# Kernel tuning notes

Hardware: AMD Instinct MI355X
Metric: run time of the kernel (lower is better)

Reference implementation:

```python
import jax, jax.numpy as jnp
import numpy as np

N_NODES = 100000
N_EDGES = 600000
N_GRAPHS = 5000
IN_DIM = 11
HID = 128
EDGE_DIM = 3
N_REST = 4  # layers 1..4
BN_EPS = 1e-5


def setup_inputs() -> dict:
    key = jax.random.key(0)
    ks = iter(jax.random.split(key, 40))
    s = 0.05
    inp = {}
    inp['x'] = jax.random.normal(next(ks), (N_NODES, IN_DIM), dtype=jnp.float32)
    inp['edge_attr'] = jax.random.normal(next(ks), (N_EDGES, EDGE_DIM), dtype=jnp.float32)
    # layer 0 (input_dim -> hidden)
    inp['e_w0'] = jax.random.normal(next(ks), (EDGE_DIM, IN_DIM), dtype=jnp.float32) * s
    inp['e_b0'] = jnp.zeros((IN_DIM,), jnp.float32)
    inp['w1_0'] = jax.random.normal(next(ks), (IN_DIM, HID), dtype=jnp.float32) * s
    inp['b1_0'] = jnp.zeros((HID,), jnp.float32)
    inp['w2_0'] = jax.random.normal(next(ks), (HID, HID), dtype=jnp.float32) * s
    inp['b2_0'] = jnp.zeros((HID,), jnp.float32)
    inp['gamma0'] = jnp.ones((HID,), jnp.float32)
    inp['beta0'] = jnp.zeros((HID,), jnp.float32)
    inp['eps0'] = jnp.zeros((), jnp.float32)
    # layers 1..4 stacked
    inp['e_w'] = jax.random.normal(next(ks), (N_REST, EDGE_DIM, HID), dtype=jnp.float32) * s
    inp['e_b'] = jnp.zeros((N_REST, HID), jnp.float32)
    inp['w1'] = jax.random.normal(next(ks), (N_REST, HID, HID), dtype=jnp.float32) * s
    inp['b1'] = jnp.zeros((N_REST, HID), jnp.float32)
    inp['w2'] = jax.random.normal(next(ks), (N_REST, HID, HID), dtype=jnp.float32) * s
    inp['b2'] = jnp.zeros((N_REST, HID), jnp.float32)
    inp['gamma'] = jnp.ones((N_REST, HID), jnp.float32)
    inp['beta'] = jnp.zeros((N_REST, HID), jnp.float32)
    inp['eps_r'] = jnp.zeros((N_REST,), jnp.float32)
    # head MLP
    inp['hw1'] = jax.random.normal(next(ks), (HID, HID), dtype=jnp.float32) * s
    inp['hb1'] = jnp.zeros((HID,), jnp.float32)
    inp['hw2'] = jax.random.normal(next(ks), (HID, HID), dtype=jnp.float32) * s
    inp['hb2'] = jnp.zeros((HID,), jnp.float32)
    inp['hw3'] = jax.random.normal(next(ks), (HID, 1), dtype=jnp.float32) * s
    inp['hb3'] = jnp.zeros((1,), jnp.float32)
    # graph structure (int constants)
    inp['edge_index'] = jax.random.randint(next(ks), (2, N_EDGES), 0, N_NODES, dtype=jnp.int32)
    inp['batch'] = jnp.sort(jax.random.randint(next(ks), (N_NODES,), 0, N_GRAPHS, dtype=jnp.int32))
    return inp


def _gine_layer(x, src, dst, edge_attr, e_w, e_b, eps, w1, b1, w2, b2, gamma, beta):
    # message = relu(x_j + Linear(edge_attr)); aggregate = scatter-add on dst
    msg = jax.nn.relu(x[src] + edge_attr @ e_w + e_b)            # [E, d]
    aggr = jax.ops.segment_sum(msg, dst, num_segments=N_NODES)  # [N, d]
    h = (1.0 + eps) * x + aggr
    h = jax.nn.relu(h @ w1 + b1) @ w2 + b2                       # GIN MLP
    mu = h.mean(axis=0)
    var = h.var(axis=0)  # biased, as torch BN training-mode normalization
    h = (h - mu) * jax.lax.rsqrt(var + BN_EPS) * gamma + beta
    return jax.nn.relu(h)


def reference(x, edge_attr, e_w0, e_b0, w1_0, b1_0, w2_0, b2_0, gamma0, beta0, eps0,
              e_w, e_b, w1, b1, w2, b2, gamma, beta, eps_r,
              hw1, hb1, hw2, hb2, hw3, hb3, edge_index, batch):
    src, dst = edge_index[0], edge_index[1]
    # layer 0: input_dim -> hidden, no residual (dims differ)
    h = _gine_layer(x, src, dst, edge_attr, e_w0, e_b0, eps0,
                    w1_0, b1_0, w2_0, b2_0, gamma0, beta0)
    # layers 1..4: hidden -> hidden, with residual
    for i in range(N_REST):
        h_res = h
        h = _gine_layer(h, src, dst, edge_attr, e_w[i], e_b[i], eps_r[i],
                        w1[i], b1[i], w2[i], b2[i], gamma[i], beta[i])
        h = h + h_res
    # global mean pool per graph
    sums = jax.ops.segment_sum(h, batch, num_segments=N_GRAPHS)
    cnts = jax.ops.segment_sum(jnp.ones((h.shape[0],), h.dtype), batch, num_segments=N_GRAPHS)
    pooled = sums / jnp.maximum(cnts, 1.0)[:, None]
    # head MLP (dropout = eval no-op)
    z = jax.nn.relu(pooled @ hw1 + hb1)
    z = jax.nn.relu(z @ hw2 + hb2)
    return z @ hw3 + hb3
```

## Files before the change

### kernel.cpp

```cpp
#include <hip/hip_runtime.h>
#include <hip/hip_fp16.h>

#define N_NODES 100000
#define N_EDGES 600000
#define N_GRAPHS 5000
#define IN_DIM 11
#define HID 128
#define NREST 4
#define BN_EPS 1e-5f
#define SCAN_BS 256
#define NBLK ((N_NODES + SCAN_BS - 1) / SCAN_BS)
#define WSLOT 16384

typedef __bf16 bf16x8 __attribute__((ext_vector_type(8)));
typedef float f32x4 __attribute__((ext_vector_type(4)));

__device__ inline bf16x8 as_bf16x8(uint4 u) { return __builtin_bit_cast(bf16x8, u); }

__device__ inline void split_bf16(float x, unsigned short& hi, unsigned short& lo) {
    unsigned int b = __float_as_uint(x);
    hi = (unsigned short)(b >> 16);
    float rem = x - __uint_as_float(b & 0xFFFF0000u);
    lo = (unsigned short)(__float_as_uint(rem) >> 16);
}

__device__ inline uint4 pack8(const unsigned short* h) {
    uint4 u;
    u.x = (unsigned)h[0] | ((unsigned)h[1] << 16);
    u.y = (unsigned)h[2] | ((unsigned)h[3] << 16);
    u.z = (unsigned)h[4] | ((unsigned)h[5] << 16);
    u.w = (unsigned)h[6] | ((unsigned)h[7] << 16);
    return u;
}

__global__ void k_zero(int* deg, int* gstart, int* gend, float* stats) {
    int i = blockIdx.x * 256 + threadIdx.x;
    if (i < N_NODES) deg[i] = 0;
    if (i < N_GRAPHS) { gstart[i] = 0; gend[i] = 0; }
    if (i < 5 * 2 * HID) stats[i] = 0.f;
}

__global__ void k_deg(const int* __restrict__ ei, int* __restrict__ deg) {
    int e = blockIdx.x * 256 + threadIdx.x;
    if (e < N_EDGES) atomicAdd(&deg[ei[N_EDGES + e]], 1);
}

__global__ void k_scan_a(const int* __restrict__ deg, int* __restrict__ rowstart,
                         int* __restrict__ bsum) {
    __shared__ int sh[SCAN_BS];
    int t = threadIdx.x, i = blockIdx.x * SCAN_BS + t;
    int v = (i < N_NODES) ? deg[i] : 0;
    sh[t] = v;
    __syncthreads();
    for (int off = 1; off < SCAN_BS; off <<= 1) {
        int add = (t >= off) ? sh[t - off] : 0;
        __syncthreads();
        sh[t] += add;
        __syncthreads();
    }
    if (i < N_NODES) rowstart[i] = sh[t] - v;
    if (t == SCAN_BS - 1) bsum[blockIdx.x] = sh[t];
}

__global__ void k_scan_b(const int* __restrict__ bsum, int* __restrict__ boff) {
    __shared__ int sh[512];
    int t = threadIdx.x;
    int v = (t < NBLK) ? bsum[t] : 0;
    sh[t] = v;
    __syncthreads();
    for (int off = 1; off < 512; off <<= 1) {
        int add = (t >= off) ? sh[t - off] : 0;
        __syncthreads();
        sh[t] += add;
        __syncthreads();
    }
    if (t < NBLK) boff[t] = sh[t] - v;
}

__global__ void k_scan_c(int* __restrict__ rowstart, const int* __restrict__ boff,
                         int* __restrict__ cur) {
    int i = blockIdx.x * 256 + threadIdx.x;
    if (i < N_NODES) {
        int v = rowstart[i] + boff[i / SCAN_BS];
        rowstart[i] = v;
        cur[i] = v;
    }
    if (i == 0) rowstart[N_NODES] = N_EDGES;
}

__global__ void k_fill(const int* __restrict__ ei, const float* __restrict__ ea,
                       int* __restrict__ cur, uint4* __restrict__ csr_pack) {
    int e = blockIdx.x * 256 + threadIdx.x;
    if (e < N_EDGES) {
        int d = ei[N_EDGES + e];
        int p = atomicAdd(&cur[d], 1);
        uint4 pk;
        pk.x = (unsigned)ei[e];
        pk.y = __float_as_uint(ea[3 * e + 0]);
        pk.z = __float_as_uint(ea[3 * e + 1]);
        pk.w = __float_as_uint(ea[3 * e + 2]);
        csr_pack[p] = pk;
    }
}

__global__ void k_pack(const float* __restrict__ w1_0, const float* __restrict__ w2_0,
                       const float* __restrict__ w1, const float* __restrict__ w2,
                       unsigned short* __restrict__ Whi, unsigned short* __restrict__ Wlo) {
    int bid = blockIdx.x;
    int slot = bid >> 5;
    int kc = (bid >> 3) & 3, cb = bid & 7;
    int lane = threadIdx.x;
    const float* src;
    int K;
    if (slot == 0) { src = w1_0; K = IN_DIM; }
    else if (slot == 1) { src = w2_0; K = HID; }
    else if (slot < 6) { src = w1 + (size_t)(slot - 2) * HID * HID; K = HID; }
    else { src = w2 + (size_t)(slot - 6) * HID * HID; K = HID; }
    int col = cb * 16 + (lane & 15);
    int kbase = kc * 32 + 8 * (lane >> 4);
    unsigned short hi[8], lo[8];
#pragma unroll
    for (int j = 0; j < 8; ++j) {
        int k = kbase + j;
        float v = (k < K) ? src[(size_t)k * HID + col] : 0.f;
        split_bf16(v, hi[j], lo[j]);
    }
    size_t base = ((size_t)bid * 64 + lane) * 8;
    *(uint4*)(Whi + base) = pack8(hi);
    *(uint4*)(Wlo + base) = pack8(lo);
}

__global__ void k_agg0(const float* __restrict__ x, const int* __restrict__ rowstart,
                       const uint4* __restrict__ csr_pack,
                       const float* __restrict__ ew, const float* __restrict__ eb,
                       const float* __restrict__ epsp, float* __restrict__ Z0) {
    int wave = (blockIdx.x * blockDim.x + threadIdx.x) >> 6;
    int lane = threadIdx.x & 63;
    if (wave >= N_NODES) return;
    int n = wave;
    int slot = lane >> 4;
    int c = lane & 15;
    int cc = (c < IN_DIM) ? c : 0;
    float w0 = ew[cc], w1 = ew[IN_DIM + cc], w2 = ew[2 * IN_DIM + cc];
    float bb = eb[cc];
    float acc = 0.f;
    int i0 = rowstart[n], i1 = rowstart[n + 1];
    for (int i = i0 + slot; i < i1; i += 4) {
        uint4 pk = csr_pack[i];
        int s = (int)pk.x;
        float m = x[s * IN_DIM + cc] + __uint_as_float(pk.y) * w0 +
                  __uint_as_float(pk.z) * w1 + __uint_as_float(pk.w) * w2 + bb;
        acc += fmaxf(m, 0.f);
    }
    acc += __shfl_xor(acc, 16, 64);
    acc += __shfl_xor(acc, 32, 64);
    if (lane < IN_DIM) {
        float epsv = 1.0f + epsp[0];
        Z0[n * IN_DIM + lane] = epsv * x[n * IN_DIM + lane] + acc;
    }
}

__global__ __launch_bounds__(256, 4) void k_agg128(
        const __half* __restrict__ hh, const int* __restrict__ rowstart,
        const uint4* __restrict__ csr_pack,
        const float* __restrict__ ew, const float* __restrict__ eb,
        const float* __restrict__ epsp, int layer, float* __restrict__ Z) {
    int wave = (blockIdx.x * blockDim.x + threadIdx.x) >> 6;
    int lane = threadIdx.x & 63;
    if (wave >= N_NODES) return;
    int n = wave;
    int slot = lane >> 4;
    int c = (lane & 15) * 8;
    float4 w0a = *(const float4*)(ew + 0 * HID + c), w0b = *(const float4*)(ew + 0 * HID + c + 4);
    float4 w1a = *(const float4*)(ew + 1 * HID + c), w1b = *(const float4*)(ew + 1 * HID + c + 4);
    float4 w2a = *(const float4*)(ew + 2 * HID + c), w2b = *(const float4*)(ew + 2 * HID + c + 4);
    float4 bba = *(const float4*)(eb + c),           bbb = *(const float4*)(eb + c + 4);
    float a0 = 0.f, a1 = 0.f, a2 = 0.f, a3 = 0.f, a4 = 0.f, a5 = 0.f, a6 = 0.f, a7 = 0.f;
    int i0 = rowstart[n], i1 = rowstart[n + 1];
    for (int i = i0 + slot; i < i1; i += 4) {
        uint4 pk = csr_pack[i];
        int s = (int)pk.x;
        float ea0 = __uint_as_float(pk.y);
        float ea1 = __uint_as_float(pk.z);
        float ea2 = __uint_as_float(pk.w);
        uint4 hv = *(const uint4*)(hh + (size_t)s * HID + c);
        float2 f0 = __half22float2(__builtin_bit_cast(__half2, hv.x));
        float2 f1 = __half22float2(__builtin_bit_cast(__half2, hv.y));
        float2 f2 = __half22float2(__builtin_bit_cast(__half2, hv.z));
        float2 f3 = __half22float2(__builtin_bit_cast(__half2, hv.w));
        a0 += fmaxf(f0.x + ea0 * w0a.x + ea1 * w1a.x + ea2 * w2a.x + bba.x, 0.f);
        a1 += fmaxf(f0.y + ea0 * w0a.y + ea1 * w1a.y + ea2 * w2a.y + bba.y, 0.f);
        a2 += fmaxf(f1.x + ea0 * w0a.z + ea1 * w1a.z + ea2 * w2a.z + bba.z, 0.f);
        a3 += fmaxf(f1.y + ea0 * w0a.w + ea1 * w1a.w + ea2 * w2a.w + bba.w, 0.f);
        a4 += fmaxf(f2.x + ea0 * w0b.x + ea1 * w1b.x + ea2 * w2b.x + bbb.x, 0.f);
        a5 += fmaxf(f2.y + ea0 * w0b.y + ea1 * w1b.y + ea2 * w2b.y + bbb.y, 0.f);
        a6 += fmaxf(f3.x + ea0 * w0b.z + ea1 * w1b.z + ea2 * w2b.z + bbb.z, 0.f);
        a7 += fmaxf(f3.y + ea0 * w0b.w + ea1 * w1b.w + ea2 * w2b.w + bbb.w, 0.f);
    }
#pragma unroll
    for (int m = 16; m <= 32; m <<= 1) {
        a0 += __shfl_xor(a0, m, 64); a1 += __shfl_xor(a1, m, 64);
        a2 += __shfl_xor(a2, m, 64); a3 += __shfl_xor(a3, m, 64);
        a4 += __shfl_xor(a4, m, 64); a5 += __shfl_xor(a5, m, 64);
        a6 += __shfl_xor(a6, m, 64); a7 += __shfl_xor(a7, m, 64);
    }
    if (slot == 0) {
        float epsv = 1.0f + epsp[layer];
        uint4 hv = *(const uint4*)(hh + (size_t)n * HID + c);
        float2 f0 = __half22float2(__builtin_bit_cast(__half2, hv.x));
        float2 f1 = __half22float2(__builtin_bit_cast(__half2, hv.y));
        float2 f2 = __half22float2(__builtin_bit_cast(__half2, hv.z));
        float2 f3 = __half22float2(__builtin_bit_cast(__half2, hv.w));
        float4 za, zb;
        za.x = epsv * f0.x + a0; za.y = epsv * f0.y + a1;
        za.z = epsv * f1.x + a2; za.w = epsv * f1.y + a3;
        zb.x = epsv * f2.x + a4; zb.y = epsv * f2.y + a5;
        zb.z = epsv * f3.x + a6; zb.w = epsv * f3.y + a7;
        *(float4*)(Z + (size_t)n * HID + c) = za;
        *(float4*)(Z + (size_t)n * HID + c + 4) = zb;
    }
}

template <int K1>
__global__ __launch_bounds__(512, 8) void k_mlp(const float* Zin,
        const unsigned short* __restrict__ W1hi, const unsigned short* __restrict__ W1lo,
        const unsigned short* __restrict__ W2hi, const unsigned short* __restrict__ W2lo,
        const float* __restrict__ B1, const float* __restrict__ B2,
        float* Hpre, float* __restrict__ stats) {
    constexpr int KC1 = (K1 == 128) ? 4 : 1;
    __shared__ __align__(16) unsigned short ahi[4 * 4 * 64 * 8];
    __shared__ __align__(16) unsigned short alo[4 * 4 * 64 * 8];
    __shared__ float red[1024];
    const int tid = threadIdx.x;
    const int w = tid >> 6;
    const int l = tid & 63;
    const int row0 = blockIdx.x * 64;

    if (K1 == 128) {
#pragma unroll
        for (int it = 0; it < 2; ++it) {
            int s = tid + it * 512;
            int lane = s & 63, kc = (s >> 6) & 3, wr = s >> 8;
            int r = row0 + wr * 16 + (lane & 15);
            int k0 = kc * 32 + 8 * (lane >> 4);
            float v[8];
            if (r < N_NODES) {
                *(float4*)(v) = *(const float4*)(Zin + (size_t)r * 128 + k0);
                *(float4*)(v + 4) = *(const float4*)(Zin + (size_t)r * 128 + k0 + 4);
            } else {
#pragma unroll
                for (int j = 0; j < 8; ++j) v[j] = 0.f;
            }
            unsigned short h[8], q[8];
#pragma unroll
            for (int j = 0; j < 8; ++j) split_bf16(v[j], h[j], q[j]);
            *(uint4*)(ahi + (size_t)s * 8) = pack8(h);
            *(uint4*)(alo + (size_t)s * 8) = pack8(q);
        }
    } else {
        if (tid < 256) {
            int lane = tid & 63, wr = tid >> 6;
            int r = row0 + wr * 16 + (lane & 15);
            int k0 = 8 * (lane >> 4);
            float v[8];
#pragma unroll
            for (int j = 0; j < 8; ++j) {
                int k = k0 + j;
                v[j] = (r < N_NODES && k < IN_DIM) ? Zin[(size_t)r * IN_DIM + k] : 0.f;
            }
            unsigned short h[8], q[8];
#pragma unroll
            for (int j = 0; j < 8; ++j) split_bf16(v[j], h[j], q[j]);
            size_t s = (size_t)(wr * 4 + 0) * 64 + lane;
            *(uint4*)(ahi + s * 8) = pack8(h);
            *(uint4*)(alo + s * 8) = pack8(q);
        }
    }
    __syncthreads();

    const int cb = w;
    const f32x4 zf = {0.f, 0.f, 0.f, 0.f};

    f32x4 acc[4];
#pragma unroll
    for (int wr = 0; wr < 4; ++wr) acc[wr] = zf;

#pragma unroll
    for (int kc = 0; kc < KC1; ++kc) {
        bf16x8 bh = as_bf16x8(*(const uint4*)(W1hi + ((size_t)(kc * 8 + cb) * 64 + l) * 8));
        bf16x8 bl = as_bf16x8(*(const uint4*)(W1lo + ((size_t)(kc * 8 + cb) * 64 + l) * 8));
#pragma unroll
        for (int wr = 0; wr < 4; ++wr) {
            bf16x8 a_h = as_bf16x8(*(const uint4*)(ahi + ((size_t)(wr * 4 + kc) * 64 + l) * 8));
            bf16x8 a_l = as_bf16x8(*(const uint4*)(alo + ((size_t)(wr * 4 + kc) * 64 + l) * 8));
            acc[wr] = __builtin_amdgcn_mfma_f32_16x16x32_bf16(a_h, bh, acc[wr], 0, 0, 0);
            acc[wr] = __builtin_amdgcn_mfma_f32_16x16x32_bf16(a_l, bh, acc[wr], 0, 0, 0);
            acc[wr] = __builtin_amdgcn_mfma_f32_16x16x32_bf16(a_h, bl, acc[wr], 0, 0, 0);
        }
    }
    __syncthreads();

    {
        float b1c = B1[cb * 16 + (l & 15)];
        int cc = l & 15;
        int g = 2 * (w & 1) + (cc >> 3);
        int j = cc & 7;
        int kc2 = w >> 1;
        int rl0 = (l >> 4) * 4;
#pragma unroll
        for (int wr = 0; wr < 4; ++wr) {
#pragma unroll
            for (int r = 0; r < 4; ++r) {
                float t = fmaxf(acc[wr][r] + b1c, 0.f);
                unsigned short th, tq;
                split_bf16(t, th, tq);
                int l2 = g * 16 + rl0 + r;
                int off = ((wr * 4 + kc2) * 64 + l2) * 8 + j;
                ahi[off] = th;
                alo[off] = tq;
            }
        }
    }
    __syncthreads();

    f32x4 acc2[4];
#pragma unroll
    for (int wr = 0; wr < 4; ++wr) acc2[wr] = zf;

#pragma unroll
    for (int kc = 0; kc < 4; ++kc) {
        bf16x8 bh = as_bf16x8(*(const uint4*)(W2hi + ((size_t)(kc * 8 + cb) * 64 + l) * 8));
        bf16x8 bl = as_bf16x8(*(const uint4*)(W2lo + ((size_t)(kc * 8 + cb) * 64 + l) * 8));
#pragma unroll
        for (int wr = 0; wr < 4; ++wr) {
            bf16x8 a_h = as_bf16x8(*(const uint4*)(ahi + ((size_t)(wr * 4 + kc) * 64 + l) * 8));
            bf16x8 a_l = as_bf16x8(*(const uint4*)(alo + ((size_t)(wr * 4 + kc) * 64 + l) * 8));
            acc2[wr] = __builtin_amdgcn_mfma_f32_16x16x32_bf16(a_h, bh, acc2[wr], 0, 0, 0);
            acc2[wr] = __builtin_amdgcn_mfma_f32_16x16x32_bf16(a_l, bh, acc2[wr], 0, 0, 0);
            acc2[wr] = __builtin_amdgcn_mfma_f32_16x16x32_bf16(a_h, bl, acc2[wr], 0, 0, 0);
        }
    }

    {
        float b2c = B2[cb * 16 + (l & 15)];
        int col = cb * 16 + (l & 15);
        float s0 = 0.f, q0 = 0.f;
#pragma unroll
        for (int wr = 0; wr < 4; ++wr) {
#pragma unroll
            for (int r = 0; r < 4; ++r) {
                int grow = row0 + wr * 16 + (l >> 4) * 4 + r;
                if (grow < N_NODES) {
                    float o = acc2[wr][r] + b2c;
                    Hpre[(size_t)grow * 128 + col] = o;
                    s0 += o;
                    q0 += o * o;
                }
            }
        }
        red[w * 64 + l] = s0;
        red[512 + w * 64 + l] = q0;
    }
    __syncthreads();
    if (tid < 128) {
        int b = (tid >> 4) * 64 + (tid & 15);
        float ss = red[b] + red[b + 16] + red[b + 32] + red[b + 48];
        float qq = red[512 + b] + red[512 + b + 16] + red[512 + b + 32] + red[512 + b + 48];
        atomicAdd(&stats[tid], ss);
        atomicAdd(&stats[128 + tid], qq);
    }
}

__global__ void k_bn(const float* __restrict__ Hpre, const float* __restrict__ stats,
                     const float* __restrict__ gamma, const float* __restrict__ beta,
                     const __half* __restrict__ hprev, __half* __restrict__ hout) {
    int idx = blockIdx.x * 256 + threadIdx.x;
    const float invN = 1.f / (float)N_NODES;
    int cg = (idx & 15) * 8;
    const float* hp = Hpre + (size_t)idx * 8;
    float4 v0 = *(const float4*)(hp);
    float4 v1 = *(const float4*)(hp + 4);
    float4 s0a = *(const float4*)(stats + cg);
    float4 s0b = *(const float4*)(stats + cg + 4);
    float4 s1a = *(const float4*)(stats + 128 + cg);
    float4 s1b = *(const float4*)(stats + 128 + cg + 4);
    float4 ga = *(const float4*)(gamma + cg);
    float4 gb = *(const float4*)(gamma + cg + 4);
    float4 ba = *(const float4*)(beta + cg);
    float4 bb = *(const float4*)(beta + cg + 4);
    float vv[8] = {v0.x, v0.y, v0.z, v0.w, v1.x, v1.y, v1.z, v1.w};
    float sm[8] = {s0a.x, s0a.y, s0a.z, s0a.w, s0b.x, s0b.y, s0b.z, s0b.w};
    float sq[8] = {s1a.x, s1a.y, s1a.z, s1a.w, s1b.x, s1b.y, s1b.z, s1b.w};
    float gg[8] = {ga.x, ga.y, ga.z, ga.w, gb.x, gb.y, gb.z, gb.w};
    float be[8] = {ba.x, ba.y, ba.z, ba.w, bb.x, bb.y, bb.z, bb.w};
    float o[8];
#pragma unroll
    for (int j = 0; j < 8; ++j) {
        float mu = sm[j] * invN, var = sq[j] * invN - mu * mu;
        o[j] = fmaxf((vv[j] - mu) * rsqrtf(var + BN_EPS) * gg[j] + be[j], 0.f);
    }
    if (hprev) {
        uint4 pv = *(const uint4*)(hprev + (size_t)idx * 8);
        float2 r0 = __half22float2(__builtin_bit_cast(__half2, pv.x));
        float2 r1 = __half22float2(__builtin_bit_cast(__half2, pv.y));
        float2 r2 = __half22float2(__builtin_bit_cast(__half2, pv.z));
        float2 r3 = __half22float2(__builtin_bit_cast(__half2, pv.w));
        o[0] += r0.x; o[1] += r0.y; o[2] += r1.x; o[3] += r1.y;
        o[4] += r2.x; o[5] += r2.y; o[6] += r3.x; o[7] += r3.y;
    }
    uint4 st;
    st.x = __builtin_bit_cast(unsigned int, __floats2half2_rn(o[0], o[1]));
    st.y = __builtin_bit_cast(unsigned int, __floats2half2_rn(o[2], o[3]));
    st.z = __builtin_bit_cast(unsigned int, __floats2half2_rn(o[4], o[5]));
    st.w = __builtin_bit_cast(unsigned int, __floats2half2_rn(o[6], o[7]));
    *(uint4*)(hout + (size_t)idx * 8) = st;
}

__global__ void k_bounds(const int* __restrict__ batch, int* __restrict__ gstart,
                         int* __restrict__ gend) {
    int r = blockIdx.x * 256 + threadIdx.x;
    if (r >= N_NODES) return;
    int b = batch[r];
    if (r == 0 || batch[r - 1] != b) gstart[b] = r;
    if (r == N_NODES - 1 || batch[r + 1] != b) gend[b] = r + 1;
}

__global__ void k_pool(const __half* __restrict__ hh, const int* __restrict__ gstart,
                       const int* __restrict__ gend, float* __restrict__ pooled) {
    int wave = (blockIdx.x * blockDim.x + threadIdx.x) >> 6;
    int lane = threadIdx.x & 63;
    if (wave >= N_GRAPHS) return;
    int g = wave;
    int c = lane * 2;
    int a = gstart[g], b = gend[g];
    float ax = 0.f, ay = 0.f;
    for (int r = a; r < b; ++r) {
        __half2 v = *(const __half2*)(hh + (size_t)r * HID + c);
        float2 f = __half22float2(v);
        ax += f.x;
        ay += f.y;
    }
    float d = fmaxf((float)(b - a), 1.f);
    float2 o;
    o.x = ax / d;
    o.y = ay / d;
    *(float2*)(pooled + (size_t)g * HID + c) = o;
}

__global__ void k_head(const float* __restrict__ pooled, const float* __restrict__ hw1,
                       const float* __restrict__ hb1, const float* __restrict__ hw2,
                       const float* __restrict__ hb2, const float* __restrict__ hw3,
                       const float* __restrict__ hb3, float* __restrict__ out) {
    __shared__ float ps[2][128];
    __shared__ float t1s[2][128];
    __shared__ float red[256];
    int tid = threadIdx.x;
    int rr = tid >> 7, c = tid & 127;
    int row = blockIdx.x * 2 + rr;
    ps[rr][c] = pooled[(size_t)row * 128 + c];
    __syncthreads();
    float a = hb1[c];
    for (int k = 0; k < 128; ++k) a = fmaf(ps[rr][k], hw1[k * 128 + c], a);
    t1s[rr][c] = fmaxf(a, 0.f);
    __syncthreads();
    float b = hb2[c];
    for (int k = 0; k < 128; ++k) b = fmaf(t1s[rr][k], hw2[k * 128 + c], b);
    b = fmaxf(b, 0.f);
    red[tid] = b * hw3[c];
    for (int s = 64; s > 0; s >>= 1) {
        __syncthreads();
        if (c < s) red[tid] += red[tid + s];
    }
    __syncthreads();
    if (c == 0) out[row] = red[tid] + hb3[0];
}

extern "C" void kernel_launch(void* const* d_in, const int* in_sizes, int n_in,
                              void* d_out, int out_size, void* d_ws, size_t ws_size,
                              hipStream_t stream) {
    const float* x = (const float*)d_in[0];
    const float* edge_attr = (const float*)d_in[1];
    const float* e_w0 = (const float*)d_in[2];
    const float* e_b0 = (const float*)d_in[3];
    const float* w1_0 = (const float*)d_in[4];
    const float* b1_0 = (const float*)d_in[5];
    const float* w2_0 = (const float*)d_in[6];
    const float* b2_0 = (const float*)d_in[7];
    const float* gamma0 = (const float*)d_in[8];
    const float* beta0 = (const float*)d_in[9];
    const float* eps0 = (const float*)d_in[10];
    const float* e_w = (const float*)d_in[11];
    const float* e_b = (const float*)d_in[12];
    const float* w1 = (const float*)d_in[13];
    const float* b1 = (const float*)d_in[14];
    const float* w2 = (const float*)d_in[15];
    const float* b2 = (const float*)d_in[16];
    const float* gamma = (const float*)d_in[17];
    const float* beta = (const float*)d_in[18];
    const float* eps_r = (const float*)d_in[19];
    const float* hw1 = (const float*)d_in[20];
    const float* hb1 = (const float*)d_in[21];
    const float* hw2 = (const float*)d_in[22];
    const float* hb2 = (const float*)d_in[23];
    const float* hw3 = (const float*)d_in[24];
    const float* hb3 = (const float*)d_in[25];
    const int* edge_index = (const int*)d_in[26];
    const int* batch = (const int*)d_in[27];
    float* out = (float*)d_out;

    float* wsf = (float*)d_ws;
    size_t off = 0;
    float* ZB = wsf + off;     off += (size_t)N_NODES * HID;
    float* Z0 = wsf + off;     off += (size_t)N_NODES * IN_DIM + 4;
    float* pooled = wsf + off; off += (size_t)N_GRAPHS * HID;
    float* stats = wsf + off;  off += 5 * 2 * HID;
    __half* hhA = (__half*)(wsf + off); off += (size_t)N_NODES * HID / 2;
    __half* hhB = (__half*)(wsf + off); off += (size_t)N_NODES * HID / 2;
    int* ib = (int*)(wsf + off);
    uint4* csr_pack = (uint4*)ib;
    size_t io = 4 * (size_t)N_EDGES;
    int* deg = ib + io;      io += N_NODES;
    int* rowstart = ib + io; io += N_NODES + 4;
    int* cur = ib + io;      io += N_NODES;
    int* gstart = ib + io;   io += N_GRAPHS;
    int* gend = ib + io;     io += N_GRAPHS;
    int* bsum = ib + io;     io += 512;
    int* boff = ib + io;     io += 512;
    unsigned short* Whi = (unsigned short*)(ib + io);
    unsigned short* Wlo = Whi + 10 * WSLOT;

    const int EB = (N_EDGES + 255) / 256;
    const int NB = (N_NODES + 255) / 256;
    const int MLPB = (N_NODES + 63) / 64;
    const int BNB = (N_NODES * HID / 8) / 256;

    k_zero<<<NB, 256, 0, stream>>>(deg, gstart, gend, stats);
    k_pack<<<320, 64, 0, stream>>>(w1_0, w2_0, w1, w2, Whi, Wlo);

    k_deg<<<EB, 256, 0, stream>>>(edge_index, deg);
    k_scan_a<<<NBLK, SCAN_BS, 0, stream>>>(deg, rowstart, bsum);
    k_scan_b<<<1, 512, 0, stream>>>(bsum, boff);
    k_scan_c<<<NB, 256, 0, stream>>>(rowstart, boff, cur);
    k_fill<<<EB, 256, 0, stream>>>(edge_index, edge_attr, cur, csr_pack);

    k_agg0<<<(N_NODES * 64) / 256, 256, 0, stream>>>(x, rowstart, csr_pack, e_w0,
                                                     e_b0, eps0, Z0);
    k_mlp<IN_DIM><<<MLPB, 512, 0, stream>>>(Z0, Whi + 0 * WSLOT, Wlo + 0 * WSLOT,
                                            Whi + 1 * WSLOT, Wlo + 1 * WSLOT,
                                            b1_0, b2_0, ZB, stats);
    k_bn<<<BNB, 256, 0, stream>>>(ZB, stats, gamma0, beta0, (const __half*)nullptr, hhA);

    __half* hcur = hhA;
    __half* hnxt = hhB;
    for (int i = 0; i < NREST; ++i) {
        k_agg128<<<(N_NODES * 64) / 256, 256, 0, stream>>>(
            hcur, rowstart, csr_pack, e_w + (size_t)i * 3 * HID,
            e_b + (size_t)i * HID, eps_r, i, ZB);
        k_mlp<HID><<<MLPB, 512, 0, stream>>>(ZB, Whi + (size_t)(2 + i) * WSLOT,
                                             Wlo + (size_t)(2 + i) * WSLOT,
                                             Whi + (size_t)(6 + i) * WSLOT,
                                             Wlo + (size_t)(6 + i) * WSLOT,
                                             b1 + (size_t)i * HID, b2 + (size_t)i * HID,
                                             ZB, stats + (size_t)(i + 1) * 2 * HID);
        k_bn<<<BNB, 256, 0, stream>>>(ZB, stats + (size_t)(i + 1) * 2 * HID,
                                      gamma + (size_t)i * HID, beta + (size_t)i * HID,
                                      hcur, hnxt);
        __half* t = hcur; hcur = hnxt; hnxt = t;
    }

    k_bounds<<<NB, 256, 0, stream>>>(batch, gstart, gend);
    k_pool<<<(N_GRAPHS * 64) / 256, 256, 0, stream>>>(hcur, gstart, gend, pooled);
    k_head<<<N_GRAPHS / 2, 256, 0, stream>>>(pooled, hw1, hb1, hw2, hb2, hw3, hb3, out);
}
```

Before: 942.6 us.

## Fuse neighbor aggregation into MLP kernel, staging aggregated rows in LDS

Aggregation kernels are merged into the MLP kernel. Each block of 512 threads aggregates its 64 nodes (8 per wave) and writes the split bf16 fragments straight into shared memory, so the fp32 Z intermediate no longer makes a round trip through global memory. The MLP output is also staged through LDS and written with coalesced float4 stores. The cost is less parallelism during the gather phase, since each wave now processes 8 nodes serially. Launch bounds also drop to 4 blocks per CU, which may reduce latency hiding for the irregular gathers.

```diff
diff --git a/kernel.cpp b/kernel.cpp
--- a/kernel.cpp
+++ b/kernel.cpp
@@ -11,6 +11,7 @@
 #define SCAN_BS 256
 #define NBLK ((N_NODES + SCAN_BS - 1) / SCAN_BS)
 #define WSLOT 16384
+#define FB ((N_NODES + 63) / 64)
 
 typedef __bf16 bf16x8 __attribute__((ext_vector_type(8)));
 typedef float f32x4 __attribute__((ext_vector_type(4)));
@@ -130,150 +131,132 @@
     *(uint4*)(Wlo + base) = pack8(lo);
 }
 
-__global__ void k_agg0(const float* __restrict__ x, const int* __restrict__ rowstart,
-                       const uint4* __restrict__ csr_pack,
-                       const float* __restrict__ ew, const float* __restrict__ eb,
-                       const float* __restrict__ epsp, float* __restrict__ Z0) {
-    int wave = (blockIdx.x * blockDim.x + threadIdx.x) >> 6;
-    int lane = threadIdx.x & 63;
-    if (wave >= N_NODES) return;
-    int n = wave;
-    int slot = lane >> 4;
-    int c = lane & 15;
-    int cc = (c < IN_DIM) ? c : 0;
-    float w0 = ew[cc], w1 = ew[IN_DIM + cc], w2 = ew[2 * IN_DIM + cc];
-    float bb = eb[cc];
-    float acc = 0.f;
-    int i0 = rowstart[n], i1 = rowstart[n + 1];
-    for (int i = i0 + slot; i < i1; i += 4) {
-        uint4 pk = csr_pack[i];
-        int s = (int)pk.x;
-        float m = x[s * IN_DIM + cc] + __uint_as_float(pk.y) * w0 +
-                  __uint_as_float(pk.z) * w1 + __uint_as_float(pk.w) * w2 + bb;
-        acc += fmaxf(m, 0.f);
-    }
-    acc += __shfl_xor(acc, 16, 64);
-    acc += __shfl_xor(acc, 32, 64);
-    if (lane < IN_DIM) {
-        float epsv = 1.0f + epsp[0];
-        Z0[n * IN_DIM + lane] = epsv * x[n * IN_DIM + lane] + acc;
-    }
-}
-
-__global__ __launch_bounds__(256, 4) void k_agg128(
-        const __half* __restrict__ hh, const int* __restrict__ rowstart,
-        const uint4* __restrict__ csr_pack,
+template <int K1>
+__global__ __launch_bounds__(512, 4) void k_fused(
+        const float* __restrict__ x, const __half* __restrict__ hh,
+        const int* __restrict__ rowstart, const uint4* __restrict__ csr_pack,
         const float* __restrict__ ew, const float* __restrict__ eb,
-        const float* __restrict__ epsp, int layer, float* __restrict__ Z) {
-    int wave = (blockIdx.x * blockDim.x + threadIdx.x) >> 6;
-    int lane = threadIdx.x & 63;
-    if (wave >= N_NODES) return;
-    int n = wave;
-    int slot = lane >> 4;
-    int c = (lane & 15) * 8;
-    float4 w0a = *(const float4*)(ew + 0 * HID + c), w0b = *(const float4*)(ew + 0 * HID + c + 4);
-    float4 w1a = *(const float4*)(ew + 1 * HID + c), w1b = *(const float4*)(ew + 1 * HID + c + 4);
-    float4 w2a = *(const float4*)(ew + 2 * HID + c), w2b = *(const float4*)(ew + 2 * HID + c + 4);
-    float4 bba = *(const float4*)(eb + c),           bbb = *(const float4*)(eb + c + 4);
-    float a0 = 0.f, a1 = 0.f, a2 = 0.f, a3 = 0.f, a4 = 0.f, a5 = 0.f, a6 = 0.f, a7 = 0.f;
-    int i0 = rowstart[n], i1 = rowstart[n + 1];
-    for (int i = i0 + slot; i < i1; i += 4) {
-        uint4 pk = csr_pack[i];
-        int s = (int)pk.x;
-        float ea0 = __uint_as_float(pk.y);
-        float ea1 = __uint_as_float(pk.z);
-        float ea2 = __uint_as_float(pk.w);
-        uint4 hv = *(const uint4*)(hh + (size_t)s * HID + c);
-        float2 f0 = __half22float2(__builtin_bit_cast(__half2, hv.x));
-        float2 f1 = __half22float2(__builtin_bit_cast(__half2, hv.y));
-        float2 f2 = __half22float2(__builtin_bit_cast(__half2, hv.z));
-        float2 f3 = __half22float2(__builtin_bit_cast(__half2, hv.w));
-        a0 += fmaxf(f0.x + ea0 * w0a.x + ea1 * w1a.x + ea2 * w2a.x + bba.x, 0.f);
-        a1 += fmaxf(f0.y + ea0 * w0a.y + ea1 * w1a.y + ea2 * w2a.y + bba.y, 0.f);
-        a2 += fmaxf(f1.x + ea0 * w0a.z + ea1 * w1a.z + ea2 * w2a.z + bba.z, 0.f);
-        a3 += fmaxf(f1.y + ea0 * w0a.w + ea1 * w1a.w + ea2 * w2a.w + bba.w, 0.f);
-        a4 += fmaxf(f2.x + ea0 * w0b.x + ea1 * w1b.x + ea2 * w2b.x + bbb.x, 0.f);
-        a5 += fmaxf(f2.y + ea0 * w0b.y + ea1 * w1b.y + ea2 * w2b.y + bbb.y, 0.f);
-        a6 += fmaxf(f3.x + ea0 * w0b.z + ea1 * w1b.z + ea2 * w2b.z + bbb.z, 0.f);
-        a7 += fmaxf(f3.y + ea0 * w0b.w + ea1 * w1b.w + ea2 * w2b.w + bbb.w, 0.f);
-    }
-#pragma unroll
-    for (int m = 16; m <= 32; m <<= 1) {
-        a0 += __shfl_xor(a0, m, 64); a1 += __shfl_xor(a1, m, 64);
-        a2 += __shfl_xor(a2, m, 64); a3 += __shfl_xor(a3, m, 64);
-        a4 += __shfl_xor(a4, m, 64); a5 += __shfl_xor(a5, m, 64);
-        a6 += __shfl_xor(a6, m, 64); a7 += __shfl_xor(a7, m, 64);
-    }
-    if (slot == 0) {
-        float epsv = 1.0f + epsp[layer];
-        uint4 hv = *(const uint4*)(hh + (size_t)n * HID + c);
-        float2 f0 = __half22float2(__builtin_bit_cast(__half2, hv.x));
-        float2 f1 = __half22float2(__builtin_bit_cast(__half2, hv.y));
-        float2 f2 = __half22float2(__builtin_bit_cast(__half2, hv.z));
-        float2 f3 = __half22float2(__builtin_bit_cast(__half2, hv.w));
-        float4 za, zb;
-        za.x = epsv * f0.x + a0; za.y = epsv * f0.y + a1;
-        za.z = epsv * f1.x + a2; za.w = epsv * f1.y + a3;
-        zb.x = epsv * f2.x + a4; zb.y = epsv * f2.y + a5;
-        zb.z = epsv * f3.x + a6; zb.w = epsv * f3.y + a7;
-        *(float4*)(Z + (size_t)n * HID + c) = za;
-        *(float4*)(Z + (size_t)n * HID + c + 4) = zb;
-    }
-}
-
-template <int K1>
-__global__ __launch_bounds__(512, 8) void k_mlp(const float* Zin,
+        const float* __restrict__ epsp, int layer,
         const unsigned short* __restrict__ W1hi, const unsigned short* __restrict__ W1lo,
         const unsigned short* __restrict__ W2hi, const unsigned short* __restrict__ W2lo,
         const float* __restrict__ B1, const float* __restrict__ B2,
-        float* Hpre, float* __restrict__ stats) {
+        float* __restrict__ Hpre, float* __restrict__ stats) {
     constexpr int KC1 = (K1 == 128) ? 4 : 1;
-    __shared__ __align__(16) unsigned short ahi[4 * 4 * 64 * 8];
-    __shared__ __align__(16) unsigned short alo[4 * 4 * 64 * 8];
+    __shared__ __align__(16) unsigned short afrag[2 * 4 * 4 * 64 * 8];
     __shared__ float red[1024];
+    unsigned short* ahi = afrag;
+    unsigned short* alo = afrag + 8192;
     const int tid = threadIdx.x;
     const int w = tid >> 6;
     const int l = tid & 63;
     const int row0 = blockIdx.x * 64;
+    const float epsv = 1.0f + epsp[layer];
+    const int slot = l >> 4;
+
+    if (K1 == 11) {
+        if (tid < 256) {
+            int off = ((tid >> 6) * 256 + (tid & 63)) * 8;
+            uint4 z = {0, 0, 0, 0};
+            *(uint4*)(ahi + off) = z;
+            *(uint4*)(alo + off) = z;
+        }
+        __syncthreads();
+    }
 
     if (K1 == 128) {
-#pragma unroll
-        for (int it = 0; it < 2; ++it) {
-            int s = tid + it * 512;
-            int lane = s & 63, kc = (s >> 6) & 3, wr = s >> 8;
-            int r = row0 + wr * 16 + (lane & 15);
-            int k0 = kc * 32 + 8 * (lane >> 4);
-            float v[8];
-            if (r < N_NODES) {
-                *(float4*)(v) = *(const float4*)(Zin + (size_t)r * 128 + k0);
-                *(float4*)(v + 4) = *(const float4*)(Zin + (size_t)r * 128 + k0 + 4);
-            } else {
-#pragma unroll
-                for (int j = 0; j < 8; ++j) v[j] = 0.f;
-            }
-            unsigned short h[8], q[8];
-#pragma unroll
-            for (int j = 0; j < 8; ++j) split_bf16(v[j], h[j], q[j]);
-            *(uint4*)(ahi + (size_t)s * 8) = pack8(h);
-            *(uint4*)(alo + (size_t)s * 8) = pack8(q);
+        int cg = (l & 15) * 8;
+        float4 w0a = *(const float4*)(ew + 0 * HID + cg), w0b = *(const float4*)(ew + 0 * HID + cg + 4);
+        float4 w1a = *(const float4*)(ew + 1 * HID + cg), w1b = *(const float4*)(ew + 1 * HID + cg + 4);
+        float4 w2a = *(const float4*)(ew + 2 * HID + cg), w2b = *(const float4*)(ew + 2 * HID + cg + 4);
+        float4 bba = *(const float4*)(eb + cg),           bbb = *(const float4*)(eb + cg + 4);
+        for (int nn = 0; nn < 8; ++nn) {
+            int rl = w * 8 + nn;
+            int n = row0 + rl;
+            bool valid = (n < N_NODES);
+            float a0 = 0.f, a1 = 0.f, a2 = 0.f, a3 = 0.f, a4 = 0.f, a5 = 0.f, a6 = 0.f, a7 = 0.f;
+            if (valid) {
+                int i0 = rowstart[n], i1 = rowstart[n + 1];
+                for (int i = i0 + slot; i < i1; i += 4) {
+                    uint4 pk = csr_pack[i];
+                    int s = (int)pk.x;
+                    float ea0 = __uint_as_float(pk.y);
+                    float ea1 = __uint_as_float(pk.z);
+                    float ea2 = __uint_as_float(pk.w);
+                    uint4 hv = *(const uint4*)(hh + (size_t)s * HID + cg);
+                    float2 f0 = __half22float2(__builtin_bit_cast(__half2, hv.x));
+                    float2 f1 = __half22float2(__builtin_bit_cast(__half2, hv.y));
+                    float2 f2 = __half22float2(__builtin_bit_cast(__half2, hv.z));
+                    float2 f3 = __half22float2(__builtin_bit_cast(__half2, hv.w));
+                    a0 += fmaxf(f0.x + ea0 * w0a.x + ea1 * w1a.x + ea2 * w2a.x + bba.x, 0.f);
+                    a1 += fmaxf(f0.y + ea0 * w0a.y + ea1 * w1a.y + ea2 * w2a.y + bba.y, 0.f);
+                    a2 += fmaxf(f1.x + ea0 * w0a.z + ea1 * w1a.z + ea2 * w2a.z + bba.z, 0.f);
+                    a3 += fmaxf(f1.y + ea0 * w0a.w + ea1 * w1a.w + ea2 * w2a.w + bba.w, 0.f);
+                    a4 += fmaxf(f2.x + ea0 * w0b.x + ea1 * w1b.x + ea2 * w2b.x + bbb.x, 0.f);
+                    a5 += fmaxf(f2.y + ea0 * w0b.y + ea1 * w1b.y + ea2 * w2b.y + bbb.y, 0.f);
+                    a6 += fmaxf(f3.x + ea0 * w0b.z + ea1 * w1b.z + ea2 * w2b.z + bbb.z, 0.f);
+                    a7 += fmaxf(f3.y + ea0 * w0b.w + ea1 * w1b.w + ea2 * w2b.w + bbb.w, 0.f);
+                }
+            }
+#pragma unroll
+            for (int m = 16; m <= 32; m <<= 1) {
+                a0 += __shfl_xor(a0, m, 64); a1 += __shfl_xor(a1, m, 64);
+                a2 += __shfl_xor(a2, m, 64); a3 += __shfl_xor(a3, m, 64);
+                a4 += __shfl_xor(a4, m, 64); a5 += __shfl_xor(a5, m, 64);
+                a6 += __shfl_xor(a6, m, 64); a7 += __shfl_xor(a7, m, 64);
+            }
+            if (slot == 0) {
+                int lc = l & 15;
+                float z[8] = {0.f, 0.f, 0.f, 0.f, 0.f, 0.f, 0.f, 0.f};
+                if (valid) {
+                    uint4 hv = *(const uint4*)(hh + (size_t)n * HID + cg);
+                    float2 f0 = __half22float2(__builtin_bit_cast(__half2, hv.x));
+                    float2 f1 = __half22float2(__builtin_bit_cast(__half2, hv.y));
+                    float2 f2 = __half22float2(__builtin_bit_cast(__half2, hv.z));
+                    float2 f3 = __half22float2(__builtin_bit_cast(__half2, hv.w));
+                    z[0] = epsv * f0.x + a0; z[1] = epsv * f0.y + a1;
+                    z[2] = epsv * f1.x + a2; z[3] = epsv * f1.y + a3;
+                    z[4] = epsv * f2.x + a4; z[5] = epsv * f2.y + a5;
+                    z[6] = epsv * f3.x + a6; z[7] = epsv * f3.y + a7;
+                }
+                unsigned short h8[8], q8[8];
+#pragma unroll
+                for (int j = 0; j < 8; ++j) split_bf16(z[j], h8[j], q8[j]);
+                int sidx = ((rl >> 4) * 4 + (lc >> 2)) * 64 + (lc & 3) * 16 + (rl & 15);
+                *(uint4*)(ahi + (size_t)sidx * 8) = pack8(h8);
+                *(uint4*)(alo + (size_t)sidx * 8) = pack8(q8);
+            }
         }
     } else {
-        if (tid < 256) {
-            int lane = tid & 63, wr = tid >> 6;
-            int r = row0 + wr * 16 + (lane & 15);
-            int k0 = 8 * (lane >> 4);
-            float v[8];
-#pragma unroll
-            for (int j = 0; j < 8; ++j) {
-                int k = k0 + j;
-                v[j] = (r < N_NODES && k < IN_DIM) ? Zin[(size_t)r * IN_DIM + k] : 0.f;
-            }
-            unsigned short h[8], q[8];
-#pragma unroll
-            for (int j = 0; j < 8; ++j) split_bf16(v[j], h[j], q[j]);
-            size_t s = (size_t)(wr * 4 + 0) * 64 + lane;
-            *(uint4*)(ahi + s * 8) = pack8(h);
-            *(uint4*)(alo + s * 8) = pack8(q);
+        int c = l & 15;
+        int cc = (c < IN_DIM) ? c : 0;
+        float w0 = ew[cc], w1 = ew[IN_DIM + cc], w2 = ew[2 * IN_DIM + cc];
+        float bb = eb[cc];
+        for (int nn = 0; nn < 8; ++nn) {
+            int rl = w * 8 + nn;
+            int n = row0 + rl;
+            bool valid = (n < N_NODES);
+            float acc = 0.f;
+            if (valid) {
+                int i0 = rowstart[n], i1 = rowstart[n + 1];
+                for (int i = i0 + slot; i < i1; i += 4) {
+                    uint4 pk = csr_pack[i];
+                    int s = (int)pk.x;
+                    float m = x[s * IN_DIM + cc] + __uint_as_float(pk.y) * w0 +
+                              __uint_as_float(pk.z) * w1 + __uint_as_float(pk.w) * w2 + bb;
+                    acc += fmaxf(m, 0.f);
+                }
+            }
+            acc += __shfl_xor(acc, 16, 64);
+            acc += __shfl_xor(acc, 32, 64);
+            if (slot == 0 && c < IN_DIM && valid) {
+                float z = epsv * x[n * IN_DIM + c] + acc;
+                unsigned short zh, zq;
+                split_bf16(z, zh, zq);
+                int sidx = ((rl >> 4) * 4 + 0) * 64 + (c >> 3) * 16 + (rl & 15);
+                int off = sidx * 8 + (c & 7);
+                ahi[off] = zh;
+                alo[off] = zq;
+            }
         }
     }
     __syncthreads();
@@ -340,7 +323,9 @@
             acc2[wr] = __builtin_amdgcn_mfma_f32_16x16x32_bf16(a_h, bl, acc2[wr], 0, 0, 0);
         }
     }
-
+    __syncthreads();
+
+    float* sf = (float*)afrag;
     {
         float b2c = B2[cb * 16 + (l & 15)];
         int col = cb * 16 + (l & 15);
@@ -349,19 +334,23 @@
         for (int wr = 0; wr < 4; ++wr) {
 #pragma unroll
             for (int r = 0; r < 4; ++r) {
-                int grow = row0 + wr * 16 + (l >> 4) * 4 + r;
-                if (grow < N_NODES) {
-                    float o = acc2[wr][r] + b2c;
-                    Hpre[(size_t)grow * 128 + col] = o;
-                    s0 += o;
-                    q0 += o * o;
-                }
+                int lrow = wr * 16 + (l >> 4) * 4 + r;
+                float o = acc2[wr][r] + b2c;
+                sf[lrow * 128 + col] = o;
+                if (row0 + lrow < N_NODES) { s0 += o; q0 += o * o; }
             }
         }
         red[w * 64 + l] = s0;
         red[512 + w * 64 + l] = q0;
     }
     __syncthreads();
+#pragma unroll
+    for (int it = 0; it < 4; ++it) {
+        int fidx = tid + it * 512;
+        int lrow = fidx >> 5, c4 = (fidx & 31) * 4;
+        if (row0 + lrow < N_NODES)
+            *(float4*)(Hpre + (size_t)(row0 + lrow) * 128 + c4) = *(float4*)(sf + lrow * 128 + c4);
+    }
     if (tid < 128) {
         int b = (tid >> 4) * 64 + (tid & 15);
         float ss = red[b] + red[b + 16] + red[b + 32] + red[b + 48];
@@ -511,7 +500,6 @@
     float* wsf = (float*)d_ws;
     size_t off = 0;
     float* ZB = wsf + off;     off += (size_t)N_NODES * HID;
-    float* Z0 = wsf + off;     off += (size_t)N_NODES * IN_DIM + 4;
     float* pooled = wsf + off; off += (size_t)N_GRAPHS * HID;
     float* stats = wsf + off;  off += 5 * 2 * HID;
     __half* hhA = (__half*)(wsf + off); off += (size_t)N_NODES * HID / 2;
@@ -531,7 +519,6 @@
 
     const int EB = (N_EDGES + 255) / 256;
     const int NB = (N_NODES + 255) / 256;
-    const int MLPB = (N_NODES + 63) / 64;
     const int BNB = (N_NODES * HID / 8) / 256;
 
     k_zero<<<NB, 256, 0, stream>>>(deg, gstart, gend, stats);
@@ -543,25 +530,22 @@
     k_scan_c<<<NB, 256, 0, stream>>>(rowstart, boff, cur);
     k_fill<<<EB, 256, 0, stream>>>(edge_index, edge_attr, cur, csr_pack);
 
-    k_agg0<<<(N_NODES * 64) / 256, 256, 0, stream>>>(x, rowstart, csr_pack, e_w0,
-                                                     e_b0, eps0, Z0);
-    k_mlp<IN_DIM><<<MLPB, 512, 0, stream>>>(Z0, Whi + 0 * WSLOT, Wlo + 0 * WSLOT,
-                                            Whi + 1 * WSLOT, Wlo + 1 * WSLOT,
-                                            b1_0, b2_0, ZB, stats);
+    k_fused<IN_DIM><<<FB, 512, 0, stream>>>(
+        x, (const __half*)nullptr, rowstart, csr_pack, e_w0, e_b0, eps0, 0,
+        Whi + 0 * WSLOT, Wlo + 0 * WSLOT, Whi + 1 * WSLOT, Wlo + 1 * WSLOT,
+        b1_0, b2_0, ZB, stats);
     k_bn<<<BNB, 256, 0, stream>>>(ZB, stats, gamma0, beta0, (const __half*)nullptr, hhA);
 
     __half* hcur = hhA;
     __half* hnxt = hhB;
     for (int i = 0; i < NREST; ++i) {
-        k_agg128<<<(N_NODES * 64) / 256, 256, 0, stream>>>(
-            hcur, rowstart, csr_pack, e_w + (size_t)i * 3 * HID,
-            e_b + (size_t)i * HID, eps_r, i, ZB);
-        k_mlp<HID><<<MLPB, 512, 0, stream>>>(ZB, Whi + (size_t)(2 + i) * WSLOT,
-                                             Wlo + (size_t)(2 + i) * WSLOT,
-                                             Whi + (size_t)(6 + i) * WSLOT,
-                                             Wlo + (size_t)(6 + i) * WSLOT,
-                                             b1 + (size_t)i * HID, b2 + (size_t)i * HID,
-                                             ZB, stats + (size_t)(i + 1) * 2 * HID);
+        k_fused<HID><<<FB, 512, 0, stream>>>(
+            (const float*)nullptr, hcur, rowstart, csr_pack,
+            e_w + (size_t)i * 3 * HID, e_b + (size_t)i * HID, eps_r, i,
+            Whi + (size_t)(2 + i) * WSLOT, Wlo + (size_t)(2 + i) * WSLOT,
+            Whi + (size_t)(6 + i) * WSLOT, Wlo + (size_t)(6 + i) * WSLOT,
+            b1 + (size_t)i * HID, b2 + (size_t)i * HID, ZB,
+            stats + (size_t)(i + 1) * 2 * HID);
         k_bn<<<BNB, 256, 0, stream>>>(ZB, stats + (size_t)(i + 1) * 2 * HID,
                                       gamma + (size_t)i * HID, beta + (size_t)i * HID,
                                       hcur, hnxt);
```

Measured after the change: 847.8 us. 10.1% less time.
